# Optimization experiments

Hardware: AMD Instinct MI355X
Metric: run time of the kernel (lower is better)

Reference implementation:

```python
import jax, jax.numpy as jnp
import numpy as np

N, F, B = 4096, 2048, 2048


def setup_inputs() -> dict:
    key = jax.random.key(0)
    ks = jax.random.split(key, 11)
    s_h = 1.0 / np.sqrt(F).astype(np.float32)
    s_x = 1.0 / np.sqrt(B).astype(np.float32)
    inp = {
        "behavior": jax.random.normal(ks[0], (N, B), jnp.float32),
        "h0": jax.random.normal(ks[1], (N, F), jnp.float32),
        "c0": jax.random.normal(ks[2], (N, F), jnp.float32),
        "Wi_h": jax.random.normal(ks[3], (F, F), jnp.float32) * s_h,
        "Wi_x": jax.random.normal(ks[4], (B, F), jnp.float32) * s_x,
        "bi": jnp.zeros((F,), jnp.float32),
        "Wf_h": jax.random.normal(ks[5], (F, F), jnp.float32) * s_h,
        "Wf_x": jax.random.normal(ks[6], (B, F), jnp.float32) * s_x,
        "bf": jnp.zeros((F,), jnp.float32),
        "Wg_h": jax.random.normal(ks[7], (F, F), jnp.float32) * s_h,
        "Wg_x": jax.random.normal(ks[8], (B, F), jnp.float32) * s_x,
        "bg": jnp.zeros((F,), jnp.float32),
        "Wo_h": jax.random.normal(ks[9], (F, F), jnp.float32) * s_h,
        "Wo_x": jax.random.normal(ks[10], (B, F), jnp.float32) * s_x,
        "bo": jnp.zeros((F,), jnp.float32),
    }
    return inp


def reference(behavior, h0, c0, Wi_h, Wi_x, bi, Wf_h, Wf_x, bf,
              Wg_h, Wg_x, bg, Wo_h, Wo_x, bo):
    # Single-step LSTM cell: each gate is a two-input linear proj (h, behavior)
    def proj(Wh, Wx, b):
        return h0 @ Wh + behavior @ Wx + b  # [N, F]

    i = jax.nn.sigmoid(proj(Wi_h, Wi_x, bi))
    f = jax.nn.sigmoid(proj(Wf_h, Wf_x, bf))
    g = jnp.tanh(proj(Wg_h, Wg_x, bg))
    o = jax.nn.sigmoid(proj(Wo_h, Wo_x, bo))
    c = f * c0 + i * g
    h = o * jnp.tanh(c)
    return h
```

## Files before the change

kernel.cpp:

```cpp
#include <hip/hip_runtime.h>
#include <stdint.h>

#define N_ROWS 4096
#define F_DIM  2048
#define B_DIM  2048
#define K_DIM  4096

typedef __attribute__((ext_vector_type(8))) __bf16 bf16x8;
typedef __attribute__((ext_vector_type(4))) float  f32x4;
typedef unsigned short u16;

__device__ __forceinline__ u16 f2bf(float x) {
  unsigned int u = __float_as_uint(x);
  u += 0x7fffu + ((u >> 16) & 1u);
  return (u16)(u >> 16);
}

__device__ __forceinline__ void async_copy16(const void* g, void* l) {
  __builtin_amdgcn_global_load_lds(
      (const __attribute__((address_space(1))) void*)g,
      (__attribute__((address_space(3))) void*)l, 16, 0, 0);
}

__device__ __forceinline__ float sigmoid_f(float x) {
  return 1.0f / (1.0f + __expf(-x));
}
__device__ __forceinline__ float tanh_f(float x) {
  float e2 = __expf(2.0f * x);
  return 1.0f - 2.0f / (e2 + 1.0f);
}

__global__ __launch_bounds__(256) void pack_x_kernel(
    const float* __restrict__ h0, const float* __restrict__ behavior,
    u16* __restrict__ Xc)
{
  int tid = blockIdx.x * 256 + threadIdx.x;
  int row = tid >> 9;
  int k0  = (tid & 511) * 8;
  const float* src = (k0 < F_DIM) ? (h0 + (size_t)row * F_DIM + k0)
                                  : (behavior + (size_t)row * B_DIM + (k0 - F_DIM));
  const float4* s4 = (const float4*)src;
  float4 a = s4[0], b = s4[1];
  uint4 o;
  o.x = (unsigned)f2bf(a.x) | ((unsigned)f2bf(a.y) << 16);
  o.y = (unsigned)f2bf(a.z) | ((unsigned)f2bf(a.w) << 16);
  o.z = (unsigned)f2bf(b.x) | ((unsigned)f2bf(b.y) << 16);
  o.w = (unsigned)f2bf(b.z) | ((unsigned)f2bf(b.w) << 16);
  *(uint4*)(Xc + (size_t)tid * 8) = o;
}

__global__ __launch_bounds__(256) void pack_w_kernel(
    const float* __restrict__ wi_h, const float* __restrict__ wi_x,
    const float* __restrict__ wf_h, const float* __restrict__ wf_x,
    const float* __restrict__ wg_h, const float* __restrict__ wg_x,
    const float* __restrict__ wo_h, const float* __restrict__ wo_x,
    u16* __restrict__ WT)
{
  __shared__ float tileT[64 * 65];
  int g = blockIdx.z;
  const float* Wh = (g == 0) ? wi_h : (g == 1) ? wf_h : (g == 2) ? wg_h : wo_h;
  const float* Wx = (g == 0) ? wi_x : (g == 1) ? wf_x : (g == 2) ? wg_x : wo_x;
  int fb = blockIdx.x * 64;
  int kb = blockIdx.y * 64;
  const float* W = (kb < F_DIM) ? Wh : Wx;
  int kofs = (kb < F_DIM) ? kb : (kb - F_DIM);

  int t  = threadIdx.x;
  int c4 = t & 15;
  int kl = t >> 4;
#pragma unroll
  for (int r = 0; r < 4; ++r) {
    int k_l = kl + r * 16;
    float4 v = *(const float4*)(W + (size_t)(kofs + k_l) * F_DIM + fb + c4 * 4);
    tileT[(c4 * 4 + 0) * 65 + k_l] = v.x;
    tileT[(c4 * 4 + 1) * 65 + k_l] = v.y;
    tileT[(c4 * 4 + 2) * 65 + k_l] = v.z;
    tileT[(c4 * 4 + 3) * 65 + k_l] = v.w;
  }
  __syncthreads();
#pragma unroll
  for (int it = 0; it < 2; ++it) {
    int idx = it * 256 + t;
    int f_l = idx >> 3;
    int k8  = (idx & 7) * 8;
    const float* s = tileT + f_l * 65 + k8;
    uint4 o;
    o.x = (unsigned)f2bf(s[0]) | ((unsigned)f2bf(s[1]) << 16);
    o.y = (unsigned)f2bf(s[2]) | ((unsigned)f2bf(s[3]) << 16);
    o.z = (unsigned)f2bf(s[4]) | ((unsigned)f2bf(s[5]) << 16);
    o.w = (unsigned)f2bf(s[6]) | ((unsigned)f2bf(s[7]) << 16);
    *(uint4*)(WT + ((size_t)g * F_DIM + fb + f_l) * K_DIM + kb + k8) = o;
  }
}

__global__ __launch_bounds__(256) void lstm_gemm_kernel(
    const u16* __restrict__ Xc, const u16* __restrict__ WT,
    const float* __restrict__ c0,
    const float* __restrict__ bi, const float* __restrict__ bff,
    const float* __restrict__ bg, const float* __restrict__ bo,
    float* __restrict__ out)
{
  __shared__ u16 As[64 * 64];
  __shared__ u16 Bs[4 * 32 * 64];

  const int tid  = threadIdx.x;
  const int lane = tid & 63;
  const int wv   = tid >> 6;
  const int bm   = blockIdx.x;
  const int bn   = blockIdx.y;

  const u16* agp[2];
  const u16* bgp[4];
#pragma unroll
  for (int j = 0; j < 2; ++j) {
    int c = j * 256 + tid;
    int r = c >> 3, s = c & 7, o = s ^ (r & 7);
    agp[j] = Xc + (size_t)(bm * 64 + r) * K_DIM + o * 8;
  }
#pragma unroll
  for (int j = 0; j < 4; ++j) {
    int r = tid >> 3, s = tid & 7, o = s ^ (r & 7);
    bgp[j] = WT + ((size_t)j * F_DIM + bn * 32 + r) * K_DIM + o * 8;
  }
  const unsigned ubase = (unsigned)(tid & ~63) * 16u;

  f32x4 acc[4][2];
  const f32x4 zero = {0.f, 0.f, 0.f, 0.f};
#pragma unroll
  for (int g = 0; g < 4; ++g)
#pragma unroll
    for (int cf = 0; cf < 2; ++cf) acc[g][cf] = zero;

  const int q = lane >> 4, ln15 = lane & 15;

  for (int kt = 0; kt < 64; ++kt) {
#pragma unroll
    for (int j = 0; j < 2; ++j)
      async_copy16(agp[j], (char*)As + j * 4096 + ubase);
#pragma unroll
    for (int j = 0; j < 4; ++j)
      async_copy16(bgp[j], (char*)Bs + j * 4096 + ubase);
#pragma unroll
    for (int j = 0; j < 2; ++j) agp[j] += 64;
#pragma unroll
    for (int j = 0; j < 4; ++j) bgp[j] += 64;
    __syncthreads();

#pragma unroll
    for (int c = 0; c < 2; ++c) {
      bf16x8 af;
      {
        int m = wv * 16 + ln15;
        int o = c * 4 + q;
        int s = o ^ (m & 7);
        af = *(const bf16x8*)(As + m * 64 + s * 8);
      }
      bf16x8 bfr[4][2];
#pragma unroll
      for (int g = 0; g < 4; ++g)
#pragma unroll
        for (int cf = 0; cf < 2; ++cf) {
          int n = cf * 16 + ln15;
          int o = c * 4 + q;
          int s = o ^ (n & 7);
          bfr[g][cf] = *(const bf16x8*)(Bs + g * 2048 + n * 64 + s * 8);
        }
#pragma unroll
      for (int g = 0; g < 4; ++g)
#pragma unroll
        for (int cf = 0; cf < 2; ++cf)
          acc[g][cf] = __builtin_amdgcn_mfma_f32_16x16x32_bf16(
              af, bfr[g][cf], acc[g][cf], 0, 0, 0);
    }
    __syncthreads();
  }

#pragma unroll
  for (int cf = 0; cf < 2; ++cf) {
    int col = bn * 32 + cf * 16 + ln15;
    float b0 = bi[col], b1 = bff[col], b2 = bg[col], b3 = bo[col];
    int row0 = bm * 64 + wv * 16 + q * 4;
#pragma unroll
    for (int r = 0; r < 4; ++r) {
      size_t idx = (size_t)(row0 + r) * F_DIM + col;
      float pi = acc[0][cf][r] + b0;
      float pf = acc[1][cf][r] + b1;
      float pg = acc[2][cf][r] + b2;
      float po = acc[3][cf][r] + b3;
      float iv = sigmoid_f(pi);
      float fv = sigmoid_f(pf);
      float gv = tanh_f(pg);
      float ov = sigmoid_f(po);
      float cv = fv * c0[idx] + iv * gv;
      out[idx] = ov * tanh_f(cv);
    }
  }
}

extern "C" void kernel_launch(void* const* d_in, const int* in_sizes, int n_in,
                              void* d_out, int out_size, void* d_ws, size_t ws_size,
                              hipStream_t stream) {
  const float* behavior = (const float*)d_in[0];
  const float* h0       = (const float*)d_in[1];
  const float* c0       = (const float*)d_in[2];
  const float* Wi_h     = (const float*)d_in[3];
  const float* Wi_x     = (const float*)d_in[4];
  const float* bi       = (const float*)d_in[5];
  const float* Wf_h     = (const float*)d_in[6];
  const float* Wf_x     = (const float*)d_in[7];
  const float* bf       = (const float*)d_in[8];
  const float* Wg_h     = (const float*)d_in[9];
  const float* Wg_x     = (const float*)d_in[10];
  const float* bg       = (const float*)d_in[11];
  const float* Wo_h     = (const float*)d_in[12];
  const float* Wo_x     = (const float*)d_in[13];
  const float* bo       = (const float*)d_in[14];
  float* out = (float*)d_out;

  u16* Xc = (u16*)d_ws;
  u16* WT = Xc + (size_t)N_ROWS * K_DIM;

  pack_x_kernel<<<dim3(N_ROWS * (K_DIM / 8) / 256), 256, 0, stream>>>(h0, behavior, Xc);
  pack_w_kernel<<<dim3(F_DIM / 64, K_DIM / 64, 4), 256, 0, stream>>>(
      Wi_h, Wi_x, Wf_h, Wf_x, Wg_h, Wg_x, Wo_h, Wo_x, WT);
  lstm_gemm_kernel<<<dim3(N_ROWS / 64, F_DIM / 32), 256, 0, stream>>>(
      Xc, WT, c0, bi, bf, bg, bo, out);
}
```

Baseline: 572.3 us.

## Enlarge GEMM tile to 128x64 per gate using 32x32x16 MFMA

The fused LSTM GEMM block tile grows from 64 rows x 32 features to 128 rows x 64 features per gate. Each wave now computes a 64x32 sub-tile with 32x32x16 bf16 MFMAs instead of 16x16x32, which raises arithmetic intensity per LDS and global load and cuts redundant operand traffic. The launch bounds now ask for two blocks per CU, and the weight pack kernel switches to 32-wide feature tiles. The cost is more accumulator registers and more LDS per block, and the main loop is still single-buffered with no overlap.

```diff
diff --git a/kernel.cpp b/kernel.cpp
--- a/kernel.cpp
+++ b/kernel.cpp
@@ -6,8 +6,8 @@
 #define B_DIM  2048
 #define K_DIM  4096
 
-typedef __attribute__((ext_vector_type(8))) __bf16 bf16x8;
-typedef __attribute__((ext_vector_type(4))) float  f32x4;
+typedef __attribute__((ext_vector_type(8)))  __bf16 bf16x8;
+typedef __attribute__((ext_vector_type(16))) float  f32x16;
 typedef unsigned short u16;
 
 __device__ __forceinline__ u16 f2bf(float x) {
@@ -56,21 +56,21 @@
     const float* __restrict__ wo_h, const float* __restrict__ wo_x,
     u16* __restrict__ WT)
 {
-  __shared__ float tileT[64 * 65];
+  __shared__ float tileT[32 * 65];
   int g = blockIdx.z;
   const float* Wh = (g == 0) ? wi_h : (g == 1) ? wf_h : (g == 2) ? wg_h : wo_h;
   const float* Wx = (g == 0) ? wi_x : (g == 1) ? wf_x : (g == 2) ? wg_x : wo_x;
-  int fb = blockIdx.x * 64;
+  int fb = blockIdx.x * 32;
   int kb = blockIdx.y * 64;
   const float* W = (kb < F_DIM) ? Wh : Wx;
   int kofs = (kb < F_DIM) ? kb : (kb - F_DIM);
 
   int t  = threadIdx.x;
-  int c4 = t & 15;
-  int kl = t >> 4;
-#pragma unroll
-  for (int r = 0; r < 4; ++r) {
-    int k_l = kl + r * 16;
+  int c4 = t & 7;
+  int kr = t >> 3;
+#pragma unroll
+  for (int p = 0; p < 2; ++p) {
+    int k_l = kr + p * 32;
     float4 v = *(const float4*)(W + (size_t)(kofs + k_l) * F_DIM + fb + c4 * 4);
     tileT[(c4 * 4 + 0) * 65 + k_l] = v.x;
     tileT[(c4 * 4 + 1) * 65 + k_l] = v.y;
@@ -78,11 +78,9 @@
     tileT[(c4 * 4 + 3) * 65 + k_l] = v.w;
   }
   __syncthreads();
-#pragma unroll
-  for (int it = 0; it < 2; ++it) {
-    int idx = it * 256 + t;
-    int f_l = idx >> 3;
-    int k8  = (idx & 7) * 8;
+  {
+    int f_l = t >> 3;
+    int k8  = (t & 7) * 8;
     const float* s = tileT + f_l * 65 + k8;
     uint4 o;
     o.x = (unsigned)f2bf(s[0]) | ((unsigned)f2bf(s[1]) << 16);
@@ -93,15 +91,15 @@
   }
 }
 
-__global__ __launch_bounds__(256) void lstm_gemm_kernel(
+__global__ __launch_bounds__(256, 2) void lstm_gemm_kernel(
     const u16* __restrict__ Xc, const u16* __restrict__ WT,
     const float* __restrict__ c0,
     const float* __restrict__ bi, const float* __restrict__ bff,
     const float* __restrict__ bg, const float* __restrict__ bo,
     float* __restrict__ out)
 {
-  __shared__ u16 As[64 * 64];
-  __shared__ u16 Bs[4 * 32 * 64];
+  __shared__ u16 As[128 * 64];
+  __shared__ u16 Bs[4 * 64 * 64];
 
   const int tid  = threadIdx.x;
   const int lane = tid & 63;
@@ -109,90 +107,97 @@
   const int bm   = blockIdx.x;
   const int bn   = blockIdx.y;
 
-  const u16* agp[2];
-  const u16* bgp[4];
-#pragma unroll
-  for (int j = 0; j < 2; ++j) {
+  const int rw = wv & 1;
+  const int fh = wv >> 1;
+  const int l31  = lane & 31;
+  const int half = lane >> 5;
+
+  const u16* agp[4];
+  const u16* bgp[8];
+#pragma unroll
+  for (int j = 0; j < 4; ++j) {
     int c = j * 256 + tid;
-    int r = c >> 3, s = c & 7, o = s ^ (r & 7);
-    agp[j] = Xc + (size_t)(bm * 64 + r) * K_DIM + o * 8;
-  }
-#pragma unroll
-  for (int j = 0; j < 4; ++j) {
-    int r = tid >> 3, s = tid & 7, o = s ^ (r & 7);
-    bgp[j] = WT + ((size_t)j * F_DIM + bn * 32 + r) * K_DIM + o * 8;
-  }
+    int r = c >> 3, o = (c & 7) ^ (r & 7);
+    agp[j] = Xc + (size_t)(bm * 128 + r) * K_DIM + o * 8;
+  }
+#pragma unroll
+  for (int g = 0; g < 4; ++g)
+#pragma unroll
+    for (int jj = 0; jj < 2; ++jj) {
+      int c = jj * 256 + tid;
+      int r = c >> 3, o = (c & 7) ^ (r & 7);
+      bgp[g * 2 + jj] = WT + ((size_t)g * F_DIM + bn * 64 + r) * K_DIM + o * 8;
+    }
   const unsigned ubase = (unsigned)(tid & ~63) * 16u;
 
-  f32x4 acc[4][2];
-  const f32x4 zero = {0.f, 0.f, 0.f, 0.f};
+  f32x16 acc[4][2];
 #pragma unroll
   for (int g = 0; g < 4; ++g)
 #pragma unroll
-    for (int cf = 0; cf < 2; ++cf) acc[g][cf] = zero;
-
-  const int q = lane >> 4, ln15 = lane & 15;
+    for (int rh = 0; rh < 2; ++rh)
+#pragma unroll
+      for (int r = 0; r < 16; ++r) acc[g][rh][r] = 0.f;
 
   for (int kt = 0; kt < 64; ++kt) {
 #pragma unroll
-    for (int j = 0; j < 2; ++j)
+    for (int j = 0; j < 4; ++j)
       async_copy16(agp[j], (char*)As + j * 4096 + ubase);
 #pragma unroll
-    for (int j = 0; j < 4; ++j)
-      async_copy16(bgp[j], (char*)Bs + j * 4096 + ubase);
-#pragma unroll
-    for (int j = 0; j < 2; ++j) agp[j] += 64;
-#pragma unroll
-    for (int j = 0; j < 4; ++j) bgp[j] += 64;
+    for (int j = 0; j < 8; ++j)
+      async_copy16(bgp[j], (char*)Bs + (j >> 1) * 8192 + (j & 1) * 4096 + ubase);
+#pragma unroll
+    for (int j = 0; j < 4; ++j) agp[j] += 64;
+#pragma unroll
+    for (int j = 0; j < 8; ++j) bgp[j] += 64;
     __syncthreads();
 
 #pragma unroll
-    for (int c = 0; c < 2; ++c) {
-      bf16x8 af;
-      {
-        int m = wv * 16 + ln15;
-        int o = c * 4 + q;
-        int s = o ^ (m & 7);
-        af = *(const bf16x8*)(As + m * 64 + s * 8);
+    for (int c = 0; c < 4; ++c) {
+      const int oct = c * 2 + half;
+      const int sw  = oct ^ (l31 & 7);
+      bf16x8 af[2];
+#pragma unroll
+      for (int rh = 0; rh < 2; ++rh) {
+        int m = rw * 64 + rh * 32 + l31;
+        af[rh] = *(const bf16x8*)(As + m * 64 + sw * 8);
       }
-      bf16x8 bfr[4][2];
+      bf16x8 bfr[4];
+#pragma unroll
+      for (int g = 0; g < 4; ++g) {
+        int fl = fh * 32 + l31;
+        bfr[g] = *(const bf16x8*)(Bs + g * 4096 + fl * 64 + sw * 8);
+      }
 #pragma unroll
       for (int g = 0; g < 4; ++g)
 #pragma unroll
-        for (int cf = 0; cf < 2; ++cf) {
-          int n = cf * 16 + ln15;
-          int o = c * 4 + q;
-          int s = o ^ (n & 7);
-          bfr[g][cf] = *(const bf16x8*)(Bs + g * 2048 + n * 64 + s * 8);
-        }
-#pragma unroll
-      for (int g = 0; g < 4; ++g)
-#pragma unroll
-        for (int cf = 0; cf < 2; ++cf)
-          acc[g][cf] = __builtin_amdgcn_mfma_f32_16x16x32_bf16(
-              af, bfr[g][cf], acc[g][cf], 0, 0, 0);
+        for (int rh = 0; rh < 2; ++rh)
+          acc[g][rh] = __builtin_amdgcn_mfma_f32_32x32x16_bf16(
+              af[rh], bfr[g], acc[g][rh], 0, 0, 0);
     }
     __syncthreads();
   }
 
-#pragma unroll
-  for (int cf = 0; cf < 2; ++cf) {
-    int col = bn * 32 + cf * 16 + ln15;
-    float b0 = bi[col], b1 = bff[col], b2 = bg[col], b3 = bo[col];
-    int row0 = bm * 64 + wv * 16 + q * 4;
-#pragma unroll
-    for (int r = 0; r < 4; ++r) {
-      size_t idx = (size_t)(row0 + r) * F_DIM + col;
-      float pi = acc[0][cf][r] + b0;
-      float pf = acc[1][cf][r] + b1;
-      float pg = acc[2][cf][r] + b2;
-      float po = acc[3][cf][r] + b3;
-      float iv = sigmoid_f(pi);
-      float fv = sigmoid_f(pf);
-      float gv = tanh_f(pg);
-      float ov = sigmoid_f(po);
-      float cv = fv * c0[idx] + iv * gv;
-      out[idx] = ov * tanh_f(cv);
+  {
+    int f = bn * 64 + fh * 32 + l31;
+    float b0 = bi[f], b1 = bff[f], b2 = bg[f], b3 = bo[f];
+#pragma unroll
+    for (int rh = 0; rh < 2; ++rh) {
+      int row_base = bm * 128 + rw * 64 + rh * 32 + 4 * half;
+#pragma unroll
+      for (int r = 0; r < 16; ++r) {
+        int row = row_base + (r & 3) + 8 * (r >> 2);
+        size_t idx = (size_t)row * F_DIM + f;
+        float pi = acc[0][rh][r] + b0;
+        float pf = acc[1][rh][r] + b1;
+        float pg = acc[2][rh][r] + b2;
+        float po = acc[3][rh][r] + b3;
+        float iv = sigmoid_f(pi);
+        float fv = sigmoid_f(pf);
+        float gv = tanh_f(pg);
+        float ov = sigmoid_f(po);
+        float cv = fv * c0[idx] + iv * gv;
+        out[idx] = ov * tanh_f(cv);
+      }
     }
   }
 }
@@ -221,8 +226,8 @@
   u16* WT = Xc + (size_t)N_ROWS * K_DIM;
 
   pack_x_kernel<<<dim3(N_ROWS * (K_DIM / 8) / 256), 256, 0, stream>>>(h0, behavior, Xc);
-  pack_w_kernel<<<dim3(F_DIM / 64, K_DIM / 64, 4), 256, 0, stream>>>(
+  pack_w_kernel<<<dim3(F_DIM / 32, K_DIM / 64, 4), 256, 0, stream>>>(
       Wi_h, Wi_x, Wf_h, Wf_x, Wg_h, Wg_x, Wo_h, Wo_x, WT);
-  lstm_gemm_kernel<<<dim3(N_ROWS / 64, F_DIM / 32), 256, 0, stream>>>(
+  lstm_gemm_kernel<<<dim3(N_ROWS / 128, F_DIM / 64), 256, 0, stream>>>(
       Xc, WT, c0, bi, bf, bg, bo, out);
 }
```

New measurement: 508.8 us. 11.1% less time.
